# Performance work log

Measured on AMD Instinct MI355X. Metric: run time of the kernel, lower is better.

The kernel has to match this reference:

```python
import jax, jax.numpy as jnp
import numpy as np

STRIDES = (8, 16, 32)
NUM_CLASSES = 80
BINS = 16
TOPK = 10
W_CLS, W_IOU, W_DFL = 0.5, 7.5, 1.5
EPS = 1e-9


def make_grid(H, W, stride):
    ys, xs = jnp.meshgrid(jnp.arange(H, dtype=jnp.float32),
                          jnp.arange(W, dtype=jnp.float32), indexing='ij')
    return jnp.stack([(xs + 0.5) * stride, (ys + 0.5) * stride], -1).reshape(-1, 2)


def decode_dfl(dfl, grid, stride):
    # dfl: (B, 64, H, W), channel layout coord-major (4 coords x 16 bins)
    B, C, H, W = dfl.shape
    prob = jax.nn.softmax(dfl.reshape(B, 4, BINS, H, W), axis=2)
    proj = jnp.arange(BINS, dtype=dfl.dtype)
    dist = jnp.einsum('bkchw,c->bkhw', prob, proj)              # expected bin value
    dist = dist.transpose(0, 2, 3, 1).reshape(B, H * W, 4) * stride  # (B,N,4) ltrb px
    cx, cy = grid[:, 0], grid[:, 1]
    return jnp.stack([cx - dist[..., 0], cy - dist[..., 1],
                      cx + dist[..., 2], cy + dist[..., 3]], -1)   # (B,N,4) xyxy


def pairwise_iou(gt, pr, eps=1e-7):
    # gt (B,G,4), pr (B,N,4) -> (B,G,N)
    lt = jnp.maximum(gt[:, :, None, :2], pr[:, None, :, :2])
    rb = jnp.minimum(gt[:, :, None, 2:], pr[:, None, :, 2:])
    wh = jnp.clip(rb - lt, 0.0)
    inter = wh[..., 0] * wh[..., 1]
    ag = jnp.clip(gt[..., 2] - gt[..., 0], 0) * jnp.clip(gt[..., 3] - gt[..., 1], 0)
    ap = jnp.clip(pr[..., 2] - pr[..., 0], 0) * jnp.clip(pr[..., 3] - pr[..., 1], 0)
    return inter / (ag[:, :, None] + ap[:, None, :] - inter + eps)


def ciou(b1, b2, eps=1e-7):
    # elementwise CIoU over (...,4) xyxy boxes
    w1, h1 = b1[..., 2] - b1[..., 0], b1[..., 3] - b1[..., 1]
    w2, h2 = b2[..., 2] - b2[..., 0], b2[..., 3] - b2[..., 1]
    lt = jnp.maximum(b1[..., :2], b2[..., :2])
    rb = jnp.minimum(b1[..., 2:], b2[..., 2:])
    wh = jnp.clip(rb - lt, 0.0)
    inter = wh[..., 0] * wh[..., 1]
    union = w1 * h1 + w2 * h2 - inter + eps
    iou = inter / union
    cw = jnp.maximum(b1[..., 2], b2[..., 2]) - jnp.minimum(b1[..., 0], b2[..., 0])
    ch = jnp.maximum(b1[..., 3], b2[..., 3]) - jnp.minimum(b1[..., 1], b2[..., 1])
    c2 = cw * cw + ch * ch + eps
    rho2 = ((b1[..., 0] + b1[..., 2] - b2[..., 0] - b2[..., 2]) ** 2 +
            (b1[..., 1] + b1[..., 3] - b2[..., 1] - b2[..., 3]) ** 2) / 4.0
    v = (4.0 / np.pi ** 2) * (jnp.arctan(w2 / (h2 + eps)) - jnp.arctan(w1 / (h1 + eps))) ** 2
    a = jax.lax.stop_gradient(v / (v - iou + (1.0 + eps)))
    return iou - rho2 / c2 - a * v


def tal_assign(scores, pred_boxes, gt_bboxes, gt_labels, grid, topk=TOPK, alpha=0.5, beta=6.0):
    B, N, C = scores.shape
    G = gt_bboxes.shape[1]
    mask_gt = gt_bboxes.sum(-1) > 0                                    # (B,G) zero-padded gts
    cx, cy = grid[None, None, :, 0], grid[None, None, :, 1]
    in_gts = ((cx > gt_bboxes[..., 0:1]) & (cx < gt_bboxes[..., 2:3]) &
              (cy > gt_bboxes[..., 1:2]) & (cy < gt_bboxes[..., 3:4]))  # (B,G,N)
    iou = pairwise_iou(gt_bboxes, pred_boxes)                          # (B,G,N)
    probs = jax.nn.sigmoid(scores)                                     # (B,N,C)
    idx = jnp.broadcast_to(gt_labels[:, None, :], (B, N, G))
    cls_g = jnp.take_along_axis(probs, idx, axis=2).transpose(0, 2, 1)  # (B,G,N)
    valid = in_gts & mask_gt[:, :, None]
    align = jnp.where(valid, (cls_g ** alpha) * (iou ** beta), 0.0)
    vals, idxk = jax.lax.top_k(align, topk)                            # (B,G,K)
    bi = jnp.arange(B)[:, None, None]
    gi = jnp.arange(G)[None, :, None]
    topk_mask = jnp.zeros((B, G, N), bool).at[bi, gi, idxk].set(vals > EPS)
    mask_pos = topk_mask & valid
    # resolve anchors assigned to multiple gts: keep gt with highest IoU
    multi = mask_pos.sum(1) > 1                                        # (B,N)
    best_gt = jnp.argmax(iou, axis=1)                                  # (B,N)
    best_oh = best_gt[:, None, :] == jnp.arange(G)[None, :, None]      # (B,G,N)
    mask_pos = jnp.where(multi[:, None, :], best_oh, mask_pos)
    fg_mask = mask_pos.any(1)                                          # (B,N)
    matched = jnp.argmax(mask_pos, axis=1)                             # (B,N)
    matched_gt_inds = jnp.where(fg_mask, matched, -1)
    target_bboxes = jnp.take_along_axis(gt_bboxes, matched[:, :, None], axis=1)
    target_labels = jnp.take_along_axis(gt_labels, matched, axis=1)
    t1h = jax.nn.one_hot(target_labels, C, dtype=scores.dtype) * fg_mask[..., None]
    align_pos = align * mask_pos
    pos_align_max = align_pos.max(2, keepdims=True)                    # per-gt max metric
    pos_iou_max = (iou * mask_pos).max(2, keepdims=True)               # per-gt max overlap
    norm = (align_pos * pos_iou_max / (pos_align_max + EPS)).max(1)    # (B,N)
    target_scores = t1h * norm[..., None]
    return target_scores, target_bboxes, fg_mask, matched_gt_inds


def yolo_loss(p0, p1, p2, gt_bboxes, gt_labels):
    scores_l, dfl_l, boxes_l, grids_l = [], [], [], []
    for p, s in zip((p0, p1, p2), STRIDES):
        B, _, H, W = p.shape
        N = H * W
        dfl, cls = p[:, :64], p[:, 64:64 + NUM_CLASSES]
        grid = make_grid(H, W, s)
        boxes_l.append(decode_dfl(dfl, grid, s))
        scores_l.append(cls.transpose(0, 2, 3, 1).reshape(B, N, NUM_CLASSES))
        dfl_l.append(dfl.transpose(0, 2, 3, 1).reshape(B, N, 4, BINS))
        grids_l.append(grid)
    all_scores = jnp.concatenate(scores_l, 1)      # (B,Nt,80)
    all_dfl = jnp.concatenate(dfl_l, 1)            # (B,Nt,4,16)
    pred_boxes = jnp.concatenate(boxes_l, 1)       # (B,Nt,4)
    grid = jnp.concatenate(grids_l, 0)             # (Nt,2)
    t_scores, t_boxes, fg, matched = tal_assign(all_scores, pred_boxes, gt_bboxes, gt_labels, grid)
    fgf = fg.astype(all_scores.dtype)
    num_pos = jnp.maximum(fgf.sum(), 1.0)
    # BCE with logits, stable form, soft targets
    s = all_scores
    bce = jnp.clip(s, 0.0) - s * t_scores + jnp.log1p(jnp.exp(-jnp.abs(s)))
    loss_cls = bce.sum() / num_pos
    loss_iou = ((1.0 - ciou(pred_boxes, t_boxes)) * fgf).sum() / num_pos  # mean over positives
    # DFL soft targets (original calls _make_dfl_targets with stride=1)
    m = jnp.clip(matched, 0)
    boxes = jnp.take_along_axis(gt_bboxes, m[:, :, None], axis=1)         # (B,Nt,4)
    gcx, gcy = grid[None, :, 0], grid[None, :, 1]
    dists = jnp.stack([jnp.clip(gcx - boxes[..., 0], 0.0),
                       jnp.clip(gcy - boxes[..., 1], 0.0),
                       jnp.clip(boxes[..., 2] - gcx, 0.0),
                       jnp.clip(boxes[..., 3] - gcy, 0.0)], -1)           # (B,Nt,4)
    tb = jnp.clip(dists, 0.0, BINS - 1 - 1e-6)
    lo = jnp.floor(tb)
    a = tb - lo
    li = lo.astype(jnp.int32)
    ui = jnp.minimum(li + 1, BINS - 1)
    td = (jax.nn.one_hot(li, BINS, dtype=tb.dtype) * (1.0 - a)[..., None] +
          jax.nn.one_hot(ui, BINS, dtype=tb.dtype) * a[..., None])        # (B,Nt,4,16)
    td = td * fgf[:, :, None, None]
    lsm = jax.nn.log_softmax(all_dfl, axis=-1)
    loss_dfl = -(td * lsm).sum() / num_pos
    return jnp.stack([W_IOU * loss_iou, W_CLS * loss_cls, W_DFL * loss_dfl])


def setup_inputs() -> dict:
    key = jax.random.key(0)
    k = jax.random.split(key, 6)
    B, G = 32, 32
    p0 = jax.random.normal(k[0], (B, 144, 80, 80), jnp.float32)
    p1 = jax.random.normal(k[1], (B, 144, 40, 40), jnp.float32)
    p2 = jax.random.normal(k[2], (B, 144, 20, 20), jnp.float32)
    c = jax.random.uniform(k[3], (B, G, 2), minval=60.0, maxval=580.0)
    wh = jax.random.uniform(k[4], (B, G, 2), minval=20.0, maxval=200.0)
    gt_bboxes = jnp.concatenate([jnp.clip(c - wh / 2, 0.0, 640.0),
                                 jnp.clip(c + wh / 2, 0.0, 640.0)], -1)
    gt_labels = jax.random.randint(k[5], (B, G), 0, NUM_CLASSES)
    return {'p0': p0, 'p1': p1, 'p2': p2, 'gt_bboxes': gt_bboxes, 'gt_labels': gt_labels}


def reference(p0, p1, p2, gt_bboxes, gt_labels):
    return yolo_loss(p0, p1, p2, gt_bboxes, gt_labels)
```

## Files before the change

### kernel.cpp

```cpp
#include <hip/hip_runtime.h>
#include <hip/hip_bf16.h>

#define NB 32
#define NG 32
#define NC 80
#define NTOT 8400
#define CH 144
#define BN (NB * NTOT)

#define TILES_PER_B 132
#define NBLK1 (NB * TILES_PER_B)
#define NBLKN 33
#define NBLK3 (NBLKN * NB)

struct AInfo {
    const float* base;
    int hw;
    int off;
    float cx, cy, stride;
};

__device__ __forceinline__ AInfo anchor_info(int n, int b, const float* p0, const float* p1, const float* p2) {
    AInfo ai;
    if (n < 6400) {
        int x = n % 80, y = n / 80;
        ai.hw = 6400; ai.off = n;
        ai.cx = (x + 0.5f) * 8.0f; ai.cy = (y + 0.5f) * 8.0f; ai.stride = 8.0f;
        ai.base = p0 + (size_t)b * CH * 6400;
    } else if (n < 8000) {
        int m = n - 6400; int x = m % 40, y = m / 40;
        ai.hw = 1600; ai.off = m;
        ai.cx = (x + 0.5f) * 16.0f; ai.cy = (y + 0.5f) * 16.0f; ai.stride = 16.0f;
        ai.base = p1 + (size_t)b * CH * 1600;
    } else {
        int m = n - 8000; int x = m % 20, y = m / 20;
        ai.hw = 400; ai.off = m;
        ai.cx = (x + 0.5f) * 32.0f; ai.cy = (y + 0.5f) * 32.0f; ai.stride = 32.0f;
        ai.base = p2 + (size_t)b * CH * 400;
    }
    return ai;
}

__device__ __forceinline__ void ins10(float a[10], float v) {
    if (v > a[9]) {
        a[9] = v;
#pragma unroll
        for (int i = 8; i >= 0; i--) {
            if (a[i + 1] > a[i]) { float t = a[i]; a[i] = a[i + 1]; a[i + 1] = t; }
        }
    }
}

__device__ __forceinline__ float iou_fn(float4 gb, float4 pb, float ap) {
    float ag = fmaxf(gb.z - gb.x, 0.f) * fmaxf(gb.w - gb.y, 0.f);
    float iw = fmaxf(fminf(gb.z, pb.z) - fmaxf(gb.x, pb.x), 0.f);
    float ih = fmaxf(fminf(gb.w, pb.w) - fmaxf(gb.y, pb.y), 0.f);
    float inter = iw * ih;
    return inter / (ag + ap - inter + 1e-7f);
}

__device__ __forceinline__ float align_metric(float s, float iou) {
    float sg = 1.f / (1.f + __expf(-s));
    float i2 = iou * iou;
    return sqrtf(sg) * i2 * i2 * i2;
}

__device__ __forceinline__ float ciou_fn(float4 p, float4 t) {
    float w1 = p.z - p.x, h1 = p.w - p.y;
    float w2 = t.z - t.x, h2 = t.w - t.y;
    float iw = fmaxf(fminf(p.z, t.z) - fmaxf(p.x, t.x), 0.f);
    float ih = fmaxf(fminf(p.w, t.w) - fmaxf(p.y, t.y), 0.f);
    float inter = iw * ih;
    float un = w1 * h1 + w2 * h2 - inter + 1e-7f;
    float iou = inter / un;
    float cw = fmaxf(p.z, t.z) - fminf(p.x, t.x);
    float chh = fmaxf(p.w, t.w) - fminf(p.y, t.y);
    float c2 = cw * cw + chh * chh + 1e-7f;
    float dx = p.x + p.z - t.x - t.z, dy = p.y + p.w - t.y - t.w;
    float rho2 = (dx * dx + dy * dy) * 0.25f;
    float da = atanf(w2 / (h2 + 1e-7f)) - atanf(w1 / (h1 + 1e-7f));
    float v = 0.4052847345693511f * da * da;
    float al = v / (v - iou + 1.f + 1e-7f);
    return iou - rho2 / c2 - al * v;
}

__global__ __launch_bounds__(256) void k1_fused(
    const float* __restrict__ p0, const float* __restrict__ p1, const float* __restrict__ p2,
    float* __restrict__ pred, float* __restrict__ lse, float* __restrict__ part_bce,
    float* __restrict__ posA, float* __restrict__ posI) {
    int blk = blockIdx.x;
    if (blk == 0) {
        for (int i = threadIdx.x; i < NB * NG; i += 256) { posA[i] = 0.f; posI[i] = 0.f; }
    }
    int b = blk / TILES_PER_B;
    int tile = blk - b * TILES_PER_B;
    const float* base; int hw, o0, lvl_off, W; float spx;
    if (tile < 100)      { base = p0; hw = 6400; o0 = tile * 64;          lvl_off = 0;    W = 80; spx = 8.f;  }
    else if (tile < 125) { base = p1; hw = 1600; o0 = (tile - 100) * 64;  lvl_off = 6400; W = 40; spx = 16.f; }
    else                 { base = p2; hw = 400;  o0 = (tile - 125) * 64;  lvl_off = 8000; W = 20; spx = 32.f; }
    base += (size_t)b * CH * hw;
    int valid = min(64, hw - o0);

    int a = threadIdx.x >> 2, k = threadIdx.x & 3;
    if (a < valid) {
        const float* col = base + (size_t)(k * 16) * hw + o0 + a;
        float v[16]; float mx = -1e30f;
#pragma unroll
        for (int j = 0; j < 16; j++) v[j] = col[(size_t)j * hw];
#pragma unroll
        for (int j = 0; j < 16; j++) mx = fmaxf(mx, v[j]);
        float se = 0.f, we = 0.f;
#pragma unroll
        for (int j = 0; j < 16; j++) { float e = __expf(v[j] - mx); se += e; we += e * (float)j; }
        float dist = we / se * spx;
        float lv = mx + __logf(se);
        int nl = o0 + a;
        int x = nl % W, y = nl / W;
        float cx = (x + 0.5f) * spx, cy = (y + 0.5f) * spx;
        float c = (k & 1) ? cy : cx;
        size_t ai = (size_t)b * NTOT + lvl_off + nl;
        pred[ai * 4 + k] = (k < 2) ? (c - dist) : (c + dist);
        lse[ai * 4 + k] = lv;
    }

    int wv = threadIdx.x >> 6, ln = threadIdx.x & 63;
    float bce = 0.f;
    if (ln < valid) {
        const float* cls = base + (size_t)64 * hw + o0 + ln;
        float vv[20];
#pragma unroll
        for (int it = 0; it < 20; it++) vv[it] = cls[(size_t)(wv + it * 4) * hw];
#pragma unroll
        for (int it = 0; it < 20; it++) {
            float s = vv[it];
            bce += fmaxf(s, 0.f) + __logf(1.f + __expf(-fabsf(s)));
        }
    }
#pragma unroll
    for (int off = 32; off > 0; off >>= 1) bce += __shfl_xor(bce, off, 64);
    __shared__ float red[4];
    if ((threadIdx.x & 63) == 0) red[threadIdx.x >> 6] = bce;
    __syncthreads();
    if (threadIdx.x == 0)
        part_bce[blk] = red[0] + red[1] + red[2] + red[3];
}

__global__ __launch_bounds__(256) void k2_thr(
    const float* __restrict__ p0, const float* __restrict__ p1, const float* __restrict__ p2,
    const float* __restrict__ gtb, const int* __restrict__ gtl,
    const float* __restrict__ pred, float* __restrict__ thr) {
    int g = blockIdx.x, b = blockIdx.y;
    const float* gb = gtb + (size_t)(b * NG + g) * 4;
    float gx1 = gb[0], gy1 = gb[1], gx2 = gb[2], gy2 = gb[3];
    bool vg = (gx1 + gy1 + gx2 + gy2) > 0.f;
    int label = gtl[b * NG + g];
    float4 gb4 = { gx1, gy1, gx2, gy2 };
    float top[10];
#pragma unroll
    for (int i = 0; i < 10; i++) top[i] = -1.f;
    const float4* pred4 = (const float4*)pred + (size_t)b * NTOT;
    for (int it = 0; it < 9; it++) {
        int n0 = it * 1024 + threadIdx.x;
        float4 pb[4]; float sc[4]; AInfo aii[4]; bool ok[4];
#pragma unroll
        for (int j = 0; j < 4; j++) {
            int n = n0 + j * 256;
            ok[j] = (n < NTOT);
            if (ok[j]) {
                aii[j] = anchor_info(n, b, p0, p1, p2);
                pb[j] = pred4[n];
                sc[j] = aii[j].base[(size_t)(64 + label) * aii[j].hw + aii[j].off];
            }
        }
#pragma unroll
        for (int j = 0; j < 4; j++) {
            if (!ok[j]) continue;
            float ap = fmaxf(pb[j].z - pb[j].x, 0.f) * fmaxf(pb[j].w - pb[j].y, 0.f);
            float iou = iou_fn(gb4, pb[j], ap);
            bool ing = (aii[j].cx > gx1) && (aii[j].cx < gx2) && (aii[j].cy > gy1) && (aii[j].cy < gy2);
            float al = 0.f;
            if (ing && vg) al = align_metric(sc[j], iou);
            ins10(top, al);
        }
    }
    __shared__ float s_top[256 * 10];
#pragma unroll
    for (int i = 0; i < 10; i++) s_top[threadIdx.x * 10 + i] = top[i];
    __syncthreads();
    if (threadIdx.x < 64) {
        float mt[10];
#pragma unroll
        for (int i = 0; i < 10; i++) mt[i] = -1.f;
        for (int src = threadIdx.x; src < 256; src += 64)
#pragma unroll
            for (int i = 0; i < 10; i++) ins10(mt, s_top[src * 10 + i]);
        float thrv = 0.f;
        for (int r = 0; r < 10; r++) {
            unsigned long long key = ((unsigned long long)__float_as_uint(mt[0]) << 32) | (unsigned)threadIdx.x;
#pragma unroll
            for (int off = 32; off > 0; off >>= 1) {
                unsigned long long o = __shfl_xor(key, off, 64);
                if (o > key) key = o;
            }
            thrv = __uint_as_float((unsigned)(key >> 32));
            if ((key & 63ULL) == (unsigned long long)threadIdx.x) {
#pragma unroll
                for (int i = 0; i < 9; i++) mt[i] = mt[i + 1];
                mt[9] = -1.f;
            }
        }
        if (threadIdx.x == 0) thr[b * NG + g] = thrv;
    }
}

__global__ __launch_bounds__(256) void k3_mask(
    const float* __restrict__ p0, const float* __restrict__ p1, const float* __restrict__ p2,
    const float* __restrict__ thr, const float* __restrict__ pred,
    const float* __restrict__ gtb, const int* __restrict__ gtl,
    unsigned* __restrict__ maskv, int* __restrict__ matchedv,
    float* __restrict__ posA, float* __restrict__ posI, unsigned* __restrict__ partN) {
    int b = blockIdx.y;
    int n = blockIdx.x * 256 + threadIdx.x;
    __shared__ float s_thr[NG];
    __shared__ float4 s_gt[NG];
    __shared__ int s_lab[NG];
    if (threadIdx.x < NG) {
        s_thr[threadIdx.x] = thr[b * NG + threadIdx.x];
        s_gt[threadIdx.x] = ((const float4*)gtb)[b * NG + threadIdx.x];
        s_lab[threadIdx.x] = gtl[b * NG + threadIdx.x];
    }
    __syncthreads();
    bool fg = false;
    if (n < NTOT) {
        AInfo ai = anchor_info(n, b, p0, p1, p2);
        float4 pb = ((const float4*)pred)[(size_t)b * NTOT + n];
        float ap = fmaxf(pb.z - pb.x, 0.f) * fmaxf(pb.w - pb.y, 0.f);
        unsigned m = 0;
#pragma unroll 8
        for (int g = 0; g < NG; g++) {
            float4 gb4 = s_gt[g];
            bool vg = (gb4.x + gb4.y + gb4.z + gb4.w) > 0.f;
            float iou = iou_fn(gb4, pb, ap);
            bool ing = (ai.cx > gb4.x) && (ai.cx < gb4.z) && (ai.cy > gb4.y) && (ai.cy < gb4.w);
            float al = 0.f;
            if (ing && vg) {
                float s = ai.base[(size_t)(64 + s_lab[g]) * ai.hw + ai.off];
                al = align_metric(s, iou);
            }
            if (al >= s_thr[g] && al > 1e-9f) m |= (1u << g);
        }
        int cnt = __popc(m);
        int matched = -1;
        if (cnt > 0) {
            if (cnt > 1) {
                float best = -1.f; int bg = 0;
                for (int g = 0; g < NG; g++) {
                    float iou = iou_fn(s_gt[g], pb, ap);
                    if (iou > best) { best = iou; bg = g; }
                }
                m = 1u << bg;
            }
            for (int g = 0; g < NG; g++) {
                if ((m >> g) & 1u) {
                    float4 gb4 = s_gt[g];
                    bool vg = (gb4.x + gb4.y + gb4.z + gb4.w) > 0.f;
                    float iou = iou_fn(gb4, pb, ap);
                    bool ing = (ai.cx > gb4.x) && (ai.cx < gb4.z) && (ai.cy > gb4.y) && (ai.cy < gb4.w);
                    float al = 0.f;
                    if (ing && vg) {
                        float s = ai.base[(size_t)(64 + s_lab[g]) * ai.hw + ai.off];
                        al = align_metric(s, iou);
                    }
                    atomicMax((int*)&posI[b * NG + g], __float_as_int(iou));
                    atomicMax((int*)&posA[b * NG + g], __float_as_int(al));
                }
            }
            matched = __ffs(m) - 1;
            fg = true;
        }
        maskv[(size_t)b * NTOT + n] = m;
        matchedv[(size_t)b * NTOT + n] = matched;
    }
    unsigned long long bal = __ballot(fg);
    __shared__ unsigned redN[4];
    if ((threadIdx.x & 63) == 0) redN[threadIdx.x >> 6] = (unsigned)__popcll(bal);
    __syncthreads();
    if (threadIdx.x == 0)
        partN[blockIdx.y * gridDim.x + blockIdx.x] = redN[0] + redN[1] + redN[2] + redN[3];
}

__global__ __launch_bounds__(256) void k5_loss(
    const float* __restrict__ p0, const float* __restrict__ p1, const float* __restrict__ p2,
    const unsigned* __restrict__ maskv, const int* __restrict__ matchedv,
    const float* __restrict__ posA, const float* __restrict__ posI,
    const float* __restrict__ gtb, const int* __restrict__ gtl,
    const float* __restrict__ pred, const float* __restrict__ lse,
    float* __restrict__ part_corr, float* __restrict__ part_liou, float* __restrict__ part_ldfl) {
    int b = blockIdx.y;
    int n = blockIdx.x * 256 + threadIdx.x;
    __shared__ float4 s_gt[NG];
    __shared__ int s_lab[NG];
    __shared__ float s_pa[NG], s_pi[NG];
    if (threadIdx.x < NG) {
        s_gt[threadIdx.x] = ((const float4*)gtb)[b * NG + threadIdx.x];
        s_lab[threadIdx.x] = gtl[b * NG + threadIdx.x];
        s_pa[threadIdx.x] = posA[b * NG + threadIdx.x];
        s_pi[threadIdx.x] = posI[b * NG + threadIdx.x];
    }
    __syncthreads();
    float corr = 0.f, liou = 0.f, ldfl = 0.f;
    if (n < NTOT) {
        int mt = matchedv[(size_t)b * NTOT + n];
        if (mt >= 0) {
            AInfo ai = anchor_info(n, b, p0, p1, p2);
            const float* base = ai.base + ai.off;
            float4 pb = ((const float4*)pred)[(size_t)b * NTOT + n];
            float ap = fmaxf(pb.z - pb.x, 0.f) * fmaxf(pb.w - pb.y, 0.f);
            unsigned m = maskv[(size_t)b * NTOT + n];
            float nrm = 0.f;
#pragma unroll 4
            for (int g = 0; g < NG; g++) {
                if ((m >> g) & 1u) {
                    float4 gb4 = s_gt[g];
                    bool vg = (gb4.x + gb4.y + gb4.z + gb4.w) > 0.f;
                    float iou = iou_fn(gb4, pb, ap);
                    bool ing = (ai.cx > gb4.x) && (ai.cx < gb4.z) && (ai.cy > gb4.y) && (ai.cy < gb4.w);
                    float al = 0.f;
                    if (ing && vg) {
                        float s = base[(size_t)(64 + s_lab[g]) * ai.hw];
                        al = align_metric(s, iou);
                    }
                    nrm = fmaxf(nrm, al * s_pi[g] / (s_pa[g] + 1e-9f));
                }
            }
            float s = base[(size_t)(64 + s_lab[mt]) * ai.hw];
            corr = s * nrm;
            float4 tb = s_gt[mt];
            liou = 1.f - ciou_fn(pb, tb);
            float4 l4 = ((const float4*)lse)[(size_t)b * NTOT + n];
            float lv[4] = { l4.x, l4.y, l4.z, l4.w };
            float d[4] = { fmaxf(ai.cx - tb.x, 0.f), fmaxf(ai.cy - tb.y, 0.f),
                           fmaxf(tb.z - ai.cx, 0.f), fmaxf(tb.w - ai.cy, 0.f) };
            float Ls[8];
            int li4[4], ui4[4]; float afr4[4];
#pragma unroll
            for (int k = 0; k < 4; k++) {
                float tbk = fminf(d[k], 14.999999f);
                float lo = floorf(tbk);
                afr4[k] = tbk - lo;
                li4[k] = (int)lo;
                ui4[k] = min(li4[k] + 1, 15);
            }
#pragma unroll
            for (int k = 0; k < 4; k++) {
                Ls[k * 2]     = base[(size_t)(k * 16 + li4[k]) * ai.hw];
                Ls[k * 2 + 1] = base[(size_t)(k * 16 + ui4[k]) * ai.hw];
            }
#pragma unroll
            for (int k = 0; k < 4; k++)
                ldfl += lv[k] - ((1.f - afr4[k]) * Ls[k * 2] + afr4[k] * Ls[k * 2 + 1]);
        }
    }
#pragma unroll
    for (int off = 32; off > 0; off >>= 1) {
        corr += __shfl_xor(corr, off, 64);
        liou += __shfl_xor(liou, off, 64);
        ldfl += __shfl_xor(ldfl, off, 64);
    }
    __shared__ float rc[4], ri[4], rd[4];
    if ((threadIdx.x & 63) == 0) {
        int w = threadIdx.x >> 6;
        rc[w] = corr; ri[w] = liou; rd[w] = ldfl;
    }
    __syncthreads();
    if (threadIdx.x == 0) {
        int blk = blockIdx.y * gridDim.x + blockIdx.x;
        part_corr[blk] = rc[0] + rc[1] + rc[2] + rc[3];
        part_liou[blk] = ri[0] + ri[1] + ri[2] + ri[3];
        part_ldfl[blk] = rd[0] + rd[1] + rd[2] + rd[3];
    }
}

__global__ __launch_bounds__(256) void k6_final(
    const float* __restrict__ part_bce, const float* __restrict__ part_corr,
    const float* __restrict__ part_liou, const float* __restrict__ part_ldfl,
    const unsigned* __restrict__ partN, float* __restrict__ out) {
    double bce = 0.0, corr = 0.0, liou = 0.0, ldfl = 0.0, np = 0.0;
    for (int i = threadIdx.x; i < NBLK1; i += 256) bce += (double)part_bce[i];
    for (int i = threadIdx.x; i < NBLK3; i += 256) {
        corr += (double)part_corr[i];
        liou += (double)part_liou[i];
        ldfl += (double)part_ldfl[i];
        np   += (double)partN[i];
    }
#pragma unroll
    for (int off = 32; off > 0; off >>= 1) {
        bce  += __shfl_xor(bce, off, 64);
        corr += __shfl_xor(corr, off, 64);
        liou += __shfl_xor(liou, off, 64);
        ldfl += __shfl_xor(ldfl, off, 64);
        np   += __shfl_xor(np, off, 64);
    }
    __shared__ double rb[4], rc[4], ri[4], rd[4], rn[4];
    if ((threadIdx.x & 63) == 0) {
        int w = threadIdx.x >> 6;
        rb[w] = bce; rc[w] = corr; ri[w] = liou; rd[w] = ldfl; rn[w] = np;
    }
    __syncthreads();
    if (threadIdx.x == 0) {
        bce  = rb[0] + rb[1] + rb[2] + rb[3];
        corr = rc[0] + rc[1] + rc[2] + rc[3];
        liou = ri[0] + ri[1] + ri[2] + ri[3];
        ldfl = rd[0] + rd[1] + rd[2] + rd[3];
        np   = rn[0] + rn[1] + rn[2] + rn[3];
        if (np < 1.0) np = 1.0;
        out[0] = (float)(7.5 * liou / np);
        out[1] = (float)(0.5 * (bce - corr) / np);
        out[2] = (float)(1.5 * ldfl / np);
    }
}

extern "C" void kernel_launch(void* const* d_in, const int* in_sizes, int n_in,
                              void* d_out, int out_size, void* d_ws, size_t ws_size,
                              hipStream_t stream) {
    const float* p0 = (const float*)d_in[0];
    const float* p1 = (const float*)d_in[1];
    const float* p2 = (const float*)d_in[2];
    const float* gtb = (const float*)d_in[3];
    const int* gtl = (const int*)d_in[4];
    float* out = (float*)d_out;

    char* w = (char*)d_ws;
    float* pred = (float*)w;
    float* lse = pred + (size_t)BN * 4;
    float* thr = lse + (size_t)BN * 4;
    float* posA = thr + NB * NG;
    float* posI = posA + NB * NG;
    unsigned* maskv = (unsigned*)(posI + NB * NG);
    int* matchedv = (int*)(maskv + BN);
    float* part_bce = (float*)(matchedv + BN);
    float* part_corr = part_bce + NBLK1;
    float* part_liou = part_corr + NBLK3;
    float* part_ldfl = part_liou + NBLK3;
    unsigned* partN = (unsigned*)(part_ldfl + NBLK3);

    hipLaunchKernelGGL(k1_fused, dim3(NBLK1), dim3(256), 0, stream,
                       p0, p1, p2, pred, lse, part_bce, posA, posI);
    hipLaunchKernelGGL(k2_thr, dim3(NG, NB), dim3(256), 0, stream,
                       p0, p1, p2, gtb, gtl, pred, thr);
    hipLaunchKernelGGL(k3_mask, dim3(NBLKN, NB), dim3(256), 0, stream,
                       p0, p1, p2, thr, pred, gtb, gtl, maskv, matchedv, posA, posI, partN);
    hipLaunchKernelGGL(k5_loss, dim3(NBLKN, NB), dim3(256), 0, stream,
                       p0, p1, p2, maskv, matchedv, posA, posI, gtb, gtl, pred, lse,
                       part_corr, part_liou, part_ldfl);
    hipLaunchKernelGGL(k6_final, dim3(1), dim3(256), 0, stream,
                       part_bce, part_corr, part_liou, part_ldfl, partN, out);
}
```

Before: 267.5 us.

## Restrict top-k scan to anchors inside GT box and vectorize class BCE loads

The threshold kernel now visits only the anchors whose centers can fall inside each GT box, using per-level grid bounds, instead of scanning all 8400 anchors per GT. The top-k buffers are initialized to zero so anchors skipped outside the box still count as zero-alignment entries. The mask kernel replaces invalid GT boxes with empty sentinel boxes and skips the IoU work when no lane in the wavefront is inside the box. The class BCE reduction switches to float4 loads, and the normalization loop walks only the set mask bits. This trades a tighter bounds computation for a large cut in redundant IoU, score loads and top-k insertions.

```diff
diff --git a/kernel.cpp b/kernel.cpp
--- a/kernel.cpp
+++ b/kernel.cpp
@@ -123,17 +123,25 @@
         lse[ai * 4 + k] = lv;
     }
 
-    int wv = threadIdx.x >> 6, ln = threadIdx.x & 63;
+    int valid4 = valid >> 2;
+    const float* clsb = base + (size_t)64 * hw + o0;
+    float4 vv[5]; bool okf[5];
+#pragma unroll
+    for (int i = 0; i < 5; i++) {
+        int u = threadIdx.x + 256 * i;
+        int ch = u >> 4, f4 = u & 15;
+        okf[i] = (f4 < valid4);
+        if (okf[i]) vv[i] = ((const float4*)(clsb + (size_t)ch * hw))[f4];
+    }
     float bce = 0.f;
-    if (ln < valid) {
-        const float* cls = base + (size_t)64 * hw + o0 + ln;
-        float vv[20];
-#pragma unroll
-        for (int it = 0; it < 20; it++) vv[it] = cls[(size_t)(wv + it * 4) * hw];
-#pragma unroll
-        for (int it = 0; it < 20; it++) {
-            float s = vv[it];
-            bce += fmaxf(s, 0.f) + __logf(1.f + __expf(-fabsf(s)));
+#pragma unroll
+    for (int i = 0; i < 5; i++) {
+        if (okf[i]) {
+            float s;
+            s = vv[i].x; bce += fmaxf(s, 0.f) + __logf(1.f + __expf(-fabsf(s)));
+            s = vv[i].y; bce += fmaxf(s, 0.f) + __logf(1.f + __expf(-fabsf(s)));
+            s = vv[i].z; bce += fmaxf(s, 0.f) + __logf(1.f + __expf(-fabsf(s)));
+            s = vv[i].w; bce += fmaxf(s, 0.f) + __logf(1.f + __expf(-fabsf(s)));
         }
     }
 #pragma unroll
@@ -155,33 +163,48 @@
     bool vg = (gx1 + gy1 + gx2 + gy2) > 0.f;
     int label = gtl[b * NG + g];
     float4 gb4 = { gx1, gy1, gx2, gy2 };
+    const float* bases[3] = { p0 + (size_t)b * CH * 6400,
+                              p1 + (size_t)b * CH * 1600,
+                              p2 + (size_t)b * CH * 400 };
+    const int Ws[3] = { 80, 40, 20 }, hws[3] = { 6400, 1600, 400 }, loff[3] = { 0, 6400, 8000 };
+    const float ss[3] = { 8.f, 16.f, 32.f };
+    int X0[3], W_[3], Y0[3], CNT[3];
+    int tot = 0;
+#pragma unroll
+    for (int l = 0; l < 3; l++) {
+        int x0 = 0, x1 = -1, y0 = 0, y1 = -1;
+        if (vg) {
+            float s = ss[l];
+            x0 = max(0, (int)floorf(gx1 / s - 0.5f));
+            x1 = min(Ws[l] - 1, (int)floorf(gx2 / s - 0.5f) + 1);
+            y0 = max(0, (int)floorf(gy1 / s - 0.5f));
+            y1 = min(Ws[l] - 1, (int)floorf(gy2 / s - 0.5f) + 1);
+        }
+        int w = x1 - x0 + 1, h = y1 - y0 + 1;
+        X0[l] = x0; Y0[l] = y0; W_[l] = w;
+        CNT[l] = (w > 0 && h > 0) ? w * h : 0;
+        tot += CNT[l];
+    }
     float top[10];
 #pragma unroll
-    for (int i = 0; i < 10; i++) top[i] = -1.f;
+    for (int i = 0; i < 10; i++) top[i] = 0.f;
     const float4* pred4 = (const float4*)pred + (size_t)b * NTOT;
-    for (int it = 0; it < 9; it++) {
-        int n0 = it * 1024 + threadIdx.x;
-        float4 pb[4]; float sc[4]; AInfo aii[4]; bool ok[4];
-#pragma unroll
-        for (int j = 0; j < 4; j++) {
-            int n = n0 + j * 256;
-            ok[j] = (n < NTOT);
-            if (ok[j]) {
-                aii[j] = anchor_info(n, b, p0, p1, p2);
-                pb[j] = pred4[n];
-                sc[j] = aii[j].base[(size_t)(64 + label) * aii[j].hw + aii[j].off];
-            }
-        }
-#pragma unroll
-        for (int j = 0; j < 4; j++) {
-            if (!ok[j]) continue;
-            float ap = fmaxf(pb[j].z - pb[j].x, 0.f) * fmaxf(pb[j].w - pb[j].y, 0.f);
-            float iou = iou_fn(gb4, pb[j], ap);
-            bool ing = (aii[j].cx > gx1) && (aii[j].cx < gx2) && (aii[j].cy > gy1) && (aii[j].cy < gy2);
-            float al = 0.f;
-            if (ing && vg) al = align_metric(sc[j], iou);
-            ins10(top, al);
-        }
+    for (int i = threadIdx.x; i < tot; i += 256) {
+        int l = 0, r = i;
+        if (r >= CNT[0]) { r -= CNT[0]; l = 1; if (r >= CNT[1]) { r -= CNT[1]; l = 2; } }
+        int w = W_[l];
+        int y = Y0[l] + r / w, x = X0[l] + r % w;
+        float s = ss[l];
+        float cx = (x + 0.5f) * s, cy = (y + 0.5f) * s;
+        int nr = y * Ws[l] + x;
+        float4 pb = pred4[loff[l] + nr];
+        float sc = bases[l][(size_t)(64 + label) * hws[l] + nr];
+        float ap = fmaxf(pb.z - pb.x, 0.f) * fmaxf(pb.w - pb.y, 0.f);
+        float iou = iou_fn(gb4, pb, ap);
+        bool ing = (cx > gx1) && (cx < gx2) && (cy > gy1) && (cy < gy2);
+        float al = 0.f;
+        if (ing && vg) al = align_metric(sc, iou);
+        ins10(top, al);
     }
     __shared__ float s_top[256 * 10];
 #pragma unroll
@@ -190,7 +213,7 @@
     if (threadIdx.x < 64) {
         float mt[10];
 #pragma unroll
-        for (int i = 0; i < 10; i++) mt[i] = -1.f;
+        for (int i = 0; i < 10; i++) mt[i] = 0.f;
         for (int src = threadIdx.x; src < 256; src += 64)
 #pragma unroll
             for (int i = 0; i < 10; i++) ins10(mt, s_top[src * 10 + i]);
@@ -206,7 +229,7 @@
             if ((key & 63ULL) == (unsigned long long)threadIdx.x) {
 #pragma unroll
                 for (int i = 0; i < 9; i++) mt[i] = mt[i + 1];
-                mt[9] = -1.f;
+                mt[9] = 0.f;
             }
         }
         if (threadIdx.x == 0) thr[b * NG + g] = thrv;
@@ -226,7 +249,10 @@
     __shared__ int s_lab[NG];
     if (threadIdx.x < NG) {
         s_thr[threadIdx.x] = thr[b * NG + threadIdx.x];
-        s_gt[threadIdx.x] = ((const float4*)gtb)[b * NG + threadIdx.x];
+        float4 gb4 = ((const float4*)gtb)[b * NG + threadIdx.x];
+        if (!((gb4.x + gb4.y + gb4.z + gb4.w) > 0.f))
+            gb4 = make_float4(1e30f, 1e30f, -1e30f, -1e30f);
+        s_gt[threadIdx.x] = gb4;
         s_lab[threadIdx.x] = gtl[b * NG + threadIdx.x];
     }
     __syncthreads();
@@ -236,18 +262,18 @@
         float4 pb = ((const float4*)pred)[(size_t)b * NTOT + n];
         float ap = fmaxf(pb.z - pb.x, 0.f) * fmaxf(pb.w - pb.y, 0.f);
         unsigned m = 0;
-#pragma unroll 8
         for (int g = 0; g < NG; g++) {
             float4 gb4 = s_gt[g];
-            bool vg = (gb4.x + gb4.y + gb4.z + gb4.w) > 0.f;
-            float iou = iou_fn(gb4, pb, ap);
             bool ing = (ai.cx > gb4.x) && (ai.cx < gb4.z) && (ai.cy > gb4.y) && (ai.cy < gb4.w);
-            float al = 0.f;
-            if (ing && vg) {
-                float s = ai.base[(size_t)(64 + s_lab[g]) * ai.hw + ai.off];
-                al = align_metric(s, iou);
-            }
-            if (al >= s_thr[g] && al > 1e-9f) m |= (1u << g);
+            if (__any(ing)) {
+                float al = 0.f;
+                if (ing) {
+                    float iou = iou_fn(gb4, pb, ap);
+                    float s = ai.base[(size_t)(64 + s_lab[g]) * ai.hw + ai.off];
+                    al = align_metric(s, iou);
+                }
+                if (al >= s_thr[g] && al > 1e-9f) m |= (1u << g);
+            }
         }
         int cnt = __popc(m);
         int matched = -1;
@@ -263,11 +289,10 @@
             for (int g = 0; g < NG; g++) {
                 if ((m >> g) & 1u) {
                     float4 gb4 = s_gt[g];
-                    bool vg = (gb4.x + gb4.y + gb4.z + gb4.w) > 0.f;
                     float iou = iou_fn(gb4, pb, ap);
                     bool ing = (ai.cx > gb4.x) && (ai.cx < gb4.z) && (ai.cy > gb4.y) && (ai.cy < gb4.w);
                     float al = 0.f;
-                    if (ing && vg) {
+                    if (ing) {
                         float s = ai.base[(size_t)(64 + s_lab[g]) * ai.hw + ai.off];
                         al = align_metric(s, iou);
                     }
@@ -318,20 +343,18 @@
             float ap = fmaxf(pb.z - pb.x, 0.f) * fmaxf(pb.w - pb.y, 0.f);
             unsigned m = maskv[(size_t)b * NTOT + n];
             float nrm = 0.f;
-#pragma unroll 4
-            for (int g = 0; g < NG; g++) {
-                if ((m >> g) & 1u) {
-                    float4 gb4 = s_gt[g];
-                    bool vg = (gb4.x + gb4.y + gb4.z + gb4.w) > 0.f;
-                    float iou = iou_fn(gb4, pb, ap);
-                    bool ing = (ai.cx > gb4.x) && (ai.cx < gb4.z) && (ai.cy > gb4.y) && (ai.cy < gb4.w);
-                    float al = 0.f;
-                    if (ing && vg) {
-                        float s = base[(size_t)(64 + s_lab[g]) * ai.hw];
-                        al = align_metric(s, iou);
-                    }
-                    nrm = fmaxf(nrm, al * s_pi[g] / (s_pa[g] + 1e-9f));
+            unsigned mm = m;
+            while (mm) {
+                int g = __ffs(mm) - 1; mm &= mm - 1;
+                float4 gb4 = s_gt[g];
+                float iou = iou_fn(gb4, pb, ap);
+                bool ing = (ai.cx > gb4.x) && (ai.cx < gb4.z) && (ai.cy > gb4.y) && (ai.cy < gb4.w);
+                float al = 0.f;
+                if (ing) {
+                    float s = base[(size_t)(64 + s_lab[g]) * ai.hw];
+                    al = align_metric(s, iou);
                 }
+                nrm = fmaxf(nrm, al * s_pi[g] / (s_pa[g] + 1e-9f));
             }
             float s = base[(size_t)(64 + s_lab[mt]) * ai.hw];
             corr = s * nrm;
```

Result: faster. 249.5 us (-6.7%).
